# Kernel optimization log

Hardware: AMD Instinct MI355X
Metric: run time of the kernel (lower is better)

The kernel has to match this reference:

```python
import jax, jax.numpy as jnp
import numpy as np

L, B, D_IN, LATENT, H_ODE = 50, 256, 256, 512, 1024
DT = 0.1  # uniform time increment per observation


def setup_inputs() -> dict:
    key = jax.random.key(0)
    ks = jax.random.split(key, 9)
    feat = jax.random.normal(ks[0], (L, B, D_IN), dtype=jnp.float32)
    tp = jnp.full((L, B, 1), DT, dtype=jnp.float32)
    data = jnp.concatenate([feat, tp], axis=-1)  # (L, B, D_IN+1)
    hid = 2 * LATENT  # GRUCell hidden size
    s_mlp1 = 1.0 / np.sqrt(LATENT)
    s_mlp2 = 1.0 / np.sqrt(H_ODE)
    s_gru_i = 1.0 / np.sqrt(hid)
    return {
        "data": data,
        # ODE func MLP: Linear(LATENT,H_ODE) -> tanh -> Linear(H_ODE,LATENT)
        "mlp_w1": jax.random.uniform(ks[1], (LATENT, H_ODE), jnp.float32, -s_mlp1, s_mlp1),
        "mlp_b1": jax.random.uniform(ks[2], (H_ODE,), jnp.float32, -s_mlp1, s_mlp1),
        "mlp_w2": jax.random.uniform(ks[3], (H_ODE, LATENT), jnp.float32, -s_mlp2, s_mlp2),
        "mlp_b2": jax.random.uniform(ks[4], (LATENT,), jnp.float32, -s_mlp2, s_mlp2),
        # GRUCell(D_IN, hid): torch layout W_ih (3*hid, D_IN), W_hh (3*hid, hid)
        "gru_wih": jax.random.uniform(ks[5], (3 * hid, D_IN), jnp.float32, -s_gru_i, s_gru_i),
        "gru_bih": jax.random.uniform(ks[6], (3 * hid,), jnp.float32, -s_gru_i, s_gru_i),
        "gru_whh": jax.random.uniform(ks[7], (3 * hid, hid), jnp.float32, -s_gru_i, s_gru_i),
        "gru_bhh": jax.random.uniform(ks[8], (3 * hid,), jnp.float32, -s_gru_i, s_gru_i),
    }


def reference(data, mlp_w1, mlp_b1, mlp_w2, mlp_b2, gru_wih, gru_bih, gru_whh, gru_bhh):
    x_seq = data[..., :-1]          # (L, B, D_IN)
    dt_seq = data[..., -1]          # (L, B) per-step time increments
    l, bs, _ = x_seq.shape
    latent = mlp_w1.shape[0]

    # With uniform dt, minimum_step = total/200 and each step uses
    # n_intermediate_tp = floor(200/L) linspace points -> n_sub Euler substeps.
    n_tp = max(2, 200 // l)
    n_sub = n_tp - 1

    def ode_f(y):
        return jnp.tanh(y @ mlp_w1 + mlp_b1) @ mlp_w2 + mlp_b2

    def gru_cell(x, h):
        gi = x @ gru_wih.T + gru_bih
        gh = h @ gru_whh.T + gru_bhh
        ir, iz, inn = jnp.split(gi, 3, axis=-1)
        hr, hz, hn = jnp.split(gh, 3, axis=-1)
        r = jax.nn.sigmoid(ir + hr)
        z = jax.nn.sigmoid(iz + hz)
        n = jnp.tanh(inn + r * hn)
        return (1.0 - z) * n + z * h

    def step(carry, inp):
        ode_state, gru_state, _ = carry
        x, dt = inp                      # x: (B, D_IN), dt: (B,)
        h_step = (dt / n_sub)[:, None]   # Euler substep size
        y = ode_state
        for _ in range(n_sub):           # fixed small unroll
            y = y + ode_f(y) * h_step
        new_h = gru_cell(x, jnp.concatenate([y, gru_state], axis=-1))
        # Original code: ode_state = new_h[..., :latent]; gru_state = new_h[..., :-latent]
        # (both are the first `latent` dims -- faithful to the source)
        new_ode = new_h[:, :latent]
        new_gru = new_h[:, :latent]
        return (new_ode, new_gru, new_h), new_ode

    zeros_lat = jnp.zeros((bs, latent), dtype=data.dtype)
    init = (zeros_lat, zeros_lat, jnp.zeros((bs, 2 * latent), dtype=data.dtype))
    (_, _, new_h), ode_states_post = jax.lax.scan(step, init, (x_seq, dt_seq))
    return ode_states_post, new_h
```

## Files before the change

kernel.cpp:

```cpp
#include <hip/hip_runtime.h>

#define LSEQ 50
#define BATCH 256
#define DIN 256
#define LAT 512
#define HID 1024
#define ROWSTRIDE 257
#define NBLK 256

typedef __attribute__((ext_vector_type(8))) short s16x8;
typedef __attribute__((ext_vector_type(4))) float f32x4;
using u16 = unsigned short;
using u64 = unsigned long long;

__device__ __forceinline__ u16 bfhi(float v) {
  union { float f; unsigned u; } a; a.f = v;
  return (u16)((a.u + 0x7FFFu + ((a.u >> 16) & 1u)) >> 16);
}
__device__ __forceinline__ void split2(float v, u16& h, u16& l) {
  u16 hu = bfhi(v);
  union { unsigned u; float f; } hf; hf.u = ((unsigned)hu) << 16;
  h = hu; l = bfhi(v - hf.f);
}
__device__ __forceinline__ float p2f(u16 h, u16 l) {
  union { unsigned u; float f; } a, b;
  a.u = ((unsigned)h) << 16; b.u = ((unsigned)l) << 16;
  return a.f + b.f;
}
__device__ __forceinline__ float sigmoidf_(float x) { return 1.f / (1.f + __expf(-x)); }
__device__ __forceinline__ f32x4 mfma16(s16x8 a, s16x8 b, f32x4 c) {
  return __builtin_amdgcn_mfma_f32_16x16x32_bf16(a, b, c, 0, 0, 0);
}
__device__ __forceinline__ f32x4 mfma3(s16x8 ah, s16x8 al, s16x8 bh, s16x8 bl, f32x4 c) {
  c = mfma16(ah, bh, c); c = mfma16(ah, bl, c); c = mfma16(al, bh, c); return c;
}
__device__ __forceinline__ ushort4 ldu4(const u16* p) { return *(const ushort4*)p; }
__device__ __forceinline__ void stu4(u16* p, ushort4 v) { *(ushort4*)p = v; }

__device__ __forceinline__ ushort4 ldu4c(const u16* p) {
  u64 v = __hip_atomic_load((const u64*)p, __ATOMIC_RELAXED, __HIP_MEMORY_SCOPE_AGENT);
  union { u64 q; ushort4 s; } u; u.q = v; return u.s;
}
__device__ __forceinline__ u16 ldu16c(const u16* p) {
  return __hip_atomic_load(p, __ATOMIC_RELAXED, __HIP_MEMORY_SCOPE_AGENT);
}
__device__ __forceinline__ void stu16c(u16* p, u16 v) {
  __hip_atomic_store(p, v, __ATOMIC_RELAXED, __HIP_MEMORY_SCOPE_AGENT);
}

__device__ __forceinline__ void kbar() {
  asm volatile("s_waitcnt lgkmcnt(0)" ::: "memory");
  __builtin_amdgcn_s_barrier();
}

__device__ __forceinline__ void slice_barrier(unsigned* line, unsigned k) {
  asm volatile("s_waitcnt vmcnt(0)" ::: "memory");
  __syncthreads();
  if (threadIdx.x == 0) {
    __hip_atomic_fetch_add(line, 1u, __ATOMIC_RELAXED, __HIP_MEMORY_SCOPE_AGENT);
    const unsigned tgt = k * 32u;
    while (__hip_atomic_load(line, __ATOMIC_RELAXED, __HIP_MEMORY_SCOPE_AGENT) < tgt) {
      __builtin_amdgcn_s_sleep(1);
    }
  }
  __syncthreads();
}

__global__ __launch_bounds__(256) void tsplit_k(const float* __restrict__ W,
    u16* __restrict__ Thi, u16* __restrict__ Tlo, int K, int N)
{
  __shared__ unsigned Ts[32][33];
  const int bk = blockIdx.x * 32, bn = blockIdx.y * 32;
  const int t = threadIdx.x;
  const int n_l = t & 31, k_l4 = (t >> 5) * 4;
  #pragma unroll
  for (int i = 0; i < 4; i++) {
    float v = W[(size_t)(bk + k_l4 + i) * N + bn + n_l];
    u16 h, l; split2(v, h, l);
    Ts[k_l4 + i][n_l] = ((unsigned)h << 16) | l;
  }
  __syncthreads();
  const int k_l = t & 31, n_l2 = t >> 5;
  #pragma unroll
  for (int i = 0; i < 4; i++) {
    int nn = n_l2 + 8 * i;
    unsigned u = Ts[k_l][nn];
    size_t o = (size_t)(bn + nn) * K + bk + k_l;
    Thi[o] = (u16)(u >> 16);
    Tlo[o] = (u16)(u & 0xFFFFu);
  }
}

__global__ __launch_bounds__(256) void esplit_k(const float* __restrict__ W,
    u16* __restrict__ Phi, u16* __restrict__ Plo)
{
  size_t i4 = ((size_t)blockIdx.x * 256 + threadIdx.x) * 4;
  float4 v = *(const float4*)&W[i4];
  u16 h[4], l[4];
  split2(v.x, h[0], l[0]); split2(v.y, h[1], l[1]);
  split2(v.z, h[2], l[2]); split2(v.w, h[3], l[3]);
  *(ushort4*)&Phi[i4] = make_ushort4(h[0], h[1], h[2], h[3]);
  *(ushort4*)&Plo[i4] = make_ushort4(l[0], l[1], l[2], l[3]);
}

__global__ __launch_bounds__(256) void init_k(u16* __restrict__ c0h, u16* __restrict__ c0l,
                                              unsigned* __restrict__ bar)
{
  size_t i4 = ((size_t)blockIdx.x * 256 + threadIdx.x) * 4;
  *(ushort4*)&c0h[i4] = make_ushort4(0, 0, 0, 0);
  *(ushort4*)&c0l[i4] = make_ushort4(0, 0, 0, 0);
  if (blockIdx.x == 0 && threadIdx.x < 16) bar[threadIdx.x * 64] = 0u;
}

template<int EPI, int NITER>
__device__ __forceinline__ void gemm_phase(
    u16* __restrict__ Sah, u16* __restrict__ Sal,
    u16* __restrict__ Sbh, u16* __restrict__ Sbl,
    const u16* __restrict__ Ahi, const u16* __restrict__ Alo, int ldA, int m0,
    const u16* __restrict__ Bhi, const u16* __restrict__ Blo, int ldB, int n0,
    const float* __restrict__ bias,
    u16* __restrict__ Ohi, u16* __restrict__ Olo,
    const float* __restrict__ data, int t, int tid)
{
  constexpr int NSEG = NITER / 4;
  const int lane = tid & 63, wave = tid >> 6;
  const int wm = (wave >> 1) << 4, wn = (wave & 1) << 4;
  const int lr = lane & 15, lq = lane >> 4;
  const int srow = tid >> 3, sk4 = (tid & 7) << 2;
  const int sidx = srow * 40 + sk4;
  const size_t rowA = (size_t)(m0 + srow) * ldA + sk4;
  const size_t rowB = (size_t)(n0 + srow) * ldB + sk4;
  const int fa = (wm + lr) * 40 + lq * 8;
  const int fb = (wn + lr) * 40 + lq * 8;
  f32x4 acc0 = {0,0,0,0}, acc1 = {0,0,0,0};

  ushort4 ah0[4], al0[4], bh0[4], bl0[4];
  ushort4 ah1[4], al1[4], bh1[4], bl1[4];

  auto load0 = [&](int seg) {
    #pragma unroll
    for (int d = 0; d < 4; ++d) {
      const int k0 = (seg * 4 + d) << 5;
      ah0[d] = ldu4c(&Ahi[rowA + k0]); al0[d] = ldu4c(&Alo[rowA + k0]);
      bh0[d] = ldu4(&Bhi[rowB + k0]);  bl0[d] = ldu4(&Blo[rowB + k0]);
    }
  };
  auto load1 = [&](int seg) {
    #pragma unroll
    for (int d = 0; d < 4; ++d) {
      const int k0 = (seg * 4 + d) << 5;
      ah1[d] = ldu4c(&Ahi[rowA + k0]); al1[d] = ldu4c(&Alo[rowA + k0]);
      bh1[d] = ldu4(&Bhi[rowB + k0]);  bl1[d] = ldu4(&Blo[rowB + k0]);
    }
  };
  auto write0 = [&]() {
    #pragma unroll
    for (int d = 0; d < 4; ++d) {
      stu4(&Sah[d * 1280 + sidx], ah0[d]); stu4(&Sal[d * 1280 + sidx], al0[d]);
      stu4(&Sbh[d * 1280 + sidx], bh0[d]); stu4(&Sbl[d * 1280 + sidx], bl0[d]);
    }
  };
  auto write1 = [&]() {
    #pragma unroll
    for (int d = 0; d < 4; ++d) {
      stu4(&Sah[5120 + d * 1280 + sidx], ah1[d]); stu4(&Sal[5120 + d * 1280 + sidx], al1[d]);
      stu4(&Sbh[5120 + d * 1280 + sidx], bh1[d]); stu4(&Sbl[5120 + d * 1280 + sidx], bl1[d]);
    }
  };
  auto compute = [&](int g) {
    #pragma unroll
    for (int d = 0; d < 4; ++d) {
      const int o = g * 5120 + d * 1280;
      s16x8 ah = *(const s16x8*)&Sah[o + fa];
      s16x8 al = *(const s16x8*)&Sal[o + fa];
      s16x8 bh = *(const s16x8*)&Sbh[o + fb];
      s16x8 bl = *(const s16x8*)&Sbl[o + fb];
      if (d & 1) acc1 = mfma3(ah, al, bh, bl, acc1);
      else       acc0 = mfma3(ah, al, bh, bl, acc0);
    }
  };

  load0(0);
  load1(1);
  write0();
  kbar();
  for (int p = 0; p < NSEG; p += 2) {
    if (p + 2 < NSEG) load0(p + 2);
    compute(0);
    write1();
    kbar();
    if (p + 3 < NSEG) load1(p + 3);
    compute(1);
    if (p + 2 < NSEG) write0();
    kbar();
  }

  #pragma unroll
  for (int r = 0; r < 4; ++r) {
    const int row = m0 + wm + lq * 4 + r;
    const int col = n0 + wn + lr;
    float v = acc0[r] + acc1[r] + bias[col];
    size_t o = (size_t)row * HID + col;
    if (EPI == 1) {
      float h1 = tanhf(v);
      u16 h, l; split2(h1, h, l);
      stu16c(&Ohi[o], h); stu16c(&Olo[o], l);
    } else {
      float dt3 = data[(size_t)(t * BATCH + row) * ROWSTRIDE + DIN] * (1.f / 3.f);
      float y = p2f(ldu16c(&Ohi[o]), ldu16c(&Olo[o])) + v * dt3;
      u16 h, l; split2(y, h, l);
      stu16c(&Ohi[o], h); stu16c(&Olo[o], l);
    }
  }
}

template<bool PLANES>
__device__ __forceinline__ void gru_phase(
    u16* pool,
    const u16* __restrict__ chi, const u16* __restrict__ clo,
    const float* __restrict__ whh, const u16* __restrict__ whhh, const u16* __restrict__ whhl,
    const float* __restrict__ wih, const u16* __restrict__ wihh, const u16* __restrict__ wihl,
    const float* __restrict__ bih, const float* __restrict__ bhh,
    const float* __restrict__ data, int t,
    u16* __restrict__ nhi, u16* __restrict__ nlo,
    float* __restrict__ out, int gc0, int m0, int tid)
{
  u16* sAh = pool;
  u16* sAl = pool + 5120;
  u16* sBh = pool + 10240;
  u16* sBl = pool + 25600;
  const int lane = tid & 63, wave = tid >> 6;
  const int wm = (wave >> 1) << 4, wn = (wave & 1) << 4;
  const int lr = lane & 15, lq = lane >> 4;
  const int srow = tid >> 3, sk4 = (tid & 7) << 2;
  const int sidx = srow * 40 + sk4;
  const int fa = (wm + lr) * 40 + lq * 8;
  const int fbn = (wn + lr) * 40 + lq * 8;
  f32x4 aR0 = {0,0,0,0}, aR1 = {0,0,0,0};
  f32x4 aZ0 = {0,0,0,0}, aZ1 = {0,0,0,0};
  f32x4 aNh0 = {0,0,0,0}, aNh1 = {0,0,0,0};
  f32x4 aNi0 = {0,0,0,0}, aNi1 = {0,0,0,0};

  {
    const size_t rowA = (size_t)(m0 + srow) * HID + sk4;
    const size_t rB0 = (size_t)(0 * 1024 + gc0 + srow) * 1024 + sk4;
    const size_t rB1 = (size_t)(1 * 1024 + gc0 + srow) * 1024 + sk4;
    const size_t rB2 = (size_t)(2 * 1024 + gc0 + srow) * 1024 + sk4;
    ushort4 Ah0[2], Al0[2], Bh0[2][3], Bl0[2][3];
    ushort4 Ah1[2], Al1[2], Bh1[2][3], Bl1[2][3];
    float4  F0[2][3], F1[2][3];

    auto load0 = [&](int seg) {
      #pragma unroll
      for (int j = 0; j < 2; ++j) {
        const int k0 = (seg * 2 + j) << 5;
        Ah0[j] = ldu4c(&chi[rowA + k0]); Al0[j] = ldu4c(&clo[rowA + k0]);
        if (PLANES) {
          Bh0[j][0] = ldu4(&whhh[rB0 + k0]); Bl0[j][0] = ldu4(&whhl[rB0 + k0]);
          Bh0[j][1] = ldu4(&whhh[rB1 + k0]); Bl0[j][1] = ldu4(&whhl[rB1 + k0]);
          Bh0[j][2] = ldu4(&whhh[rB2 + k0]); Bl0[j][2] = ldu4(&whhl[rB2 + k0]);
        } else {
          F0[j][0] = *(const float4*)&whh[rB0 + k0];
          F0[j][1] = *(const float4*)&whh[rB1 + k0];
          F0[j][2] = *(const float4*)&whh[rB2 + k0];
        }
      }
    };
    auto load1 = [&](int seg) {
      #pragma unroll
      for (int j = 0; j < 2; ++j) {
        const int k0 = (seg * 2 + j) << 5;
        Ah1[j] = ldu4c(&chi[rowA + k0]); Al1[j] = ldu4c(&clo[rowA + k0]);
        if (PLANES) {
          Bh1[j][0] = ldu4(&whhh[rB0 + k0]); Bl1[j][0] = ldu4(&whhl[rB0 + k0]);
          Bh1[j][1] = ldu4(&whhh[rB1 + k0]); Bl1[j][1] = ldu4(&whhl[rB1 + k0]);
          Bh1[j][2] = ldu4(&whhh[rB2 + k0]); Bl1[j][2] = ldu4(&whhl[rB2 + k0]);
        } else {
          F1[j][0] = *(const float4*)&whh[rB0 + k0];
          F1[j][1] = *(const float4*)&whh[rB1 + k0];
          F1[j][2] = *(const float4*)&whh[rB2 + k0];
        }
      }
    };
    auto write0 = [&]() {
      #pragma unroll
      for (int j = 0; j < 2; ++j) {
        stu4(&sAh[j * 1280 + sidx], Ah0[j]); stu4(&sAl[j * 1280 + sidx], Al0[j]);
        #pragma unroll
        for (int g = 0; g < 3; ++g) {
          if (PLANES) {
            stu4(&sBh[j * 3840 + g * 1280 + sidx], Bh0[j][g]);
            stu4(&sBl[j * 3840 + g * 1280 + sidx], Bl0[j][g]);
          } else {
            float4 w4 = F0[j][g];
            u16 h0,l0,h1,l1,h2,l2,h3,l3;
            split2(w4.x,h0,l0); split2(w4.y,h1,l1); split2(w4.z,h2,l2); split2(w4.w,h3,l3);
            stu4(&sBh[j * 3840 + g * 1280 + sidx], make_ushort4(h0,h1,h2,h3));
            stu4(&sBl[j * 3840 + g * 1280 + sidx], make_ushort4(l0,l1,l2,l3));
          }
        }
      }
    };
    auto write1 = [&]() {
      #pragma unroll
      for (int j = 0; j < 2; ++j) {
        stu4(&sAh[(2 + j) * 1280 + sidx], Ah1[j]); stu4(&sAl[(2 + j) * 1280 + sidx], Al1[j]);
        #pragma unroll
        for (int g = 0; g < 3; ++g) {
          if (PLANES) {
            stu4(&sBh[(2 + j) * 3840 + g * 1280 + sidx], Bh1[j][g]);
            stu4(&sBl[(2 + j) * 3840 + g * 1280 + sidx], Bl1[j][g]);
          } else {
            float4 w4 = F1[j][g];
            u16 h0,l0,h1,l1,h2,l2,h3,l3;
            split2(w4.x,h0,l0); split2(w4.y,h1,l1); split2(w4.z,h2,l2); split2(w4.w,h3,l3);
            stu4(&sBh[(2 + j) * 3840 + g * 1280 + sidx], make_ushort4(h0,h1,h2,h3));
            stu4(&sBl[(2 + j) * 3840 + g * 1280 + sidx], make_ushort4(l0,l1,l2,l3));
          }
        }
      }
    };
    auto compute = [&](int grp) {
      #pragma unroll
      for (int j = 0; j < 2; ++j) {
        const int slot = grp * 2 + j;
        const int sa = slot * 1280 + fa;
        const int sb = slot * 3840 + fbn;
        s16x8 ah = *(const s16x8*)&sAh[sa];
        s16x8 al = *(const s16x8*)&sAl[sa];
        #pragma unroll
        for (int g = 0; g < 3; ++g) {
          s16x8 bh = *(const s16x8*)&sBh[sb + g * 1280];
          s16x8 bl = *(const s16x8*)&sBl[sb + g * 1280];
          if (j) {
            if (g == 0) aR1 = mfma3(ah, al, bh, bl, aR1);
            else if (g == 1) aZ1 = mfma3(ah, al, bh, bl, aZ1);
            else aNh1 = mfma3(ah, al, bh, bl, aNh1);
          } else {
            if (g == 0) aR0 = mfma3(ah, al, bh, bl, aR0);
            else if (g == 1) aZ0 = mfma3(ah, al, bh, bl, aZ0);
            else aNh0 = mfma3(ah, al, bh, bl, aNh0);
          }
        }
      }
    };

    load0(0); load1(1); write0(); kbar();
    for (int p = 0; p < 16; p += 2) {
      if (p + 2 < 16) load0(p + 2);
      compute(0);
      write1();
      kbar();
      if (p + 3 < 16) load1(p + 3);
      compute(1);
      if (p + 2 < 16) write0();
      kbar();
    }
  }

  {
    const size_t rowX = (size_t)(t * BATCH + m0 + srow) * ROWSTRIDE + sk4;
    const size_t rB0 = (size_t)(0 * 1024 + gc0 + srow) * 256 + sk4;
    const size_t rB1 = (size_t)(1 * 1024 + gc0 + srow) * 256 + sk4;
    const size_t rB2 = (size_t)(2 * 1024 + gc0 + srow) * 256 + sk4;
    float4  X0[2], X1[2];
    ushort4 Bh0[2][3], Bl0[2][3], Bh1[2][3], Bl1[2][3];
    float4  F0[2][3], F1[2][3];

    auto load0 = [&](int seg) {
      #pragma unroll
      for (int j = 0; j < 2; ++j) {
        const int k0 = (seg * 2 + j) << 5;
        X0[j] = *(const float4*)&data[rowX + k0];
        if (PLANES) {
          Bh0[j][0] = ldu4(&wihh[rB0 + k0]); Bl0[j][0] = ldu4(&wihl[rB0 + k0]);
          Bh0[j][1] = ldu4(&wihh[rB1 + k0]); Bl0[j][1] = ldu4(&wihl[rB1 + k0]);
          Bh0[j][2] = ldu4(&wihh[rB2 + k0]); Bl0[j][2] = ldu4(&wihl[rB2 + k0]);
        } else {
          F0[j][0] = *(const float4*)&wih[rB0 + k0];
          F0[j][1] = *(const float4*)&wih[rB1 + k0];
          F0[j][2] = *(const float4*)&wih[rB2 + k0];
        }
      }
    };
    auto load1 = [&](int seg) {
      #pragma unroll
      for (int j = 0; j < 2; ++j) {
        const int k0 = (seg * 2 + j) << 5;
        X1[j] = *(const float4*)&data[rowX + k0];
        if (PLANES) {
          Bh1[j][0] = ldu4(&wihh[rB0 + k0]); Bl1[j][0] = ldu4(&wihl[rB0 + k0]);
          Bh1[j][1] = ldu4(&wihh[rB1 + k0]); Bl1[j][1] = ldu4(&wihl[rB1 + k0]);
          Bh1[j][2] = ldu4(&wihh[rB2 + k0]); Bl1[j][2] = ldu4(&wihl[rB2 + k0]);
        } else {
          F1[j][0] = *(const float4*)&wih[rB0 + k0];
          F1[j][1] = *(const float4*)&wih[rB1 + k0];
          F1[j][2] = *(const float4*)&wih[rB2 + k0];
        }
      }
    };
    auto writeX = [&](const float4* X, int base) {
      #pragma unroll
      for (int j = 0; j < 2; ++j) {
        u16 xh[4], xl[4];
        split2(X[j].x, xh[0], xl[0]); split2(X[j].y, xh[1], xl[1]);
        split2(X[j].z, xh[2], xl[2]); split2(X[j].w, xh[3], xl[3]);
        stu4(&sAh[(base + j) * 1280 + sidx], make_ushort4(xh[0], xh[1], xh[2], xh[3]));
        stu4(&sAl[(base + j) * 1280 + sidx], make_ushort4(xl[0], xl[1], xl[2], xl[3]));
      }
    };
    auto write0 = [&]() {
      writeX(X0, 0);
      #pragma unroll
      for (int j = 0; j < 2; ++j)
        #pragma unroll
        for (int g = 0; g < 3; ++g) {
          if (PLANES) {
            stu4(&sBh[j * 3840 + g * 1280 + sidx], Bh0[j][g]);
            stu4(&sBl[j * 3840 + g * 1280 + sidx], Bl0[j][g]);
          } else {
            float4 w4 = F0[j][g];
            u16 h0,l0,h1,l1,h2,l2,h3,l3;
            split2(w4.x,h0,l0); split2(w4.y,h1,l1); split2(w4.z,h2,l2); split2(w4.w,h3,l3);
            stu4(&sBh[j * 3840 + g * 1280 + sidx], make_ushort4(h0,h1,h2,h3));
            stu4(&sBl[j * 3840 + g * 1280 + sidx], make_ushort4(l0,l1,l2,l3));
          }
        }
    };
    auto write1 = [&]() {
      writeX(X1, 2);
      #pragma unroll
      for (int j = 0; j < 2; ++j)
        #pragma unroll
        for (int g = 0; g < 3; ++g) {
          if (PLANES) {
            stu4(&sBh[(2 + j) * 3840 + g * 1280 + sidx], Bh1[j][g]);
            stu4(&sBl[(2 + j) * 3840 + g * 1280 + sidx], Bl1[j][g]);
          } else {
            float4 w4 = F1[j][g];
            u16 h0,l0,h1,l1,h2,l2,h3,l3;
            split2(w4.x,h0,l0); split2(w4.y,h1,l1); split2(w4.z,h2,l2); split2(w4.w,h3,l3);
            stu4(&sBh[(2 + j) * 3840 + g * 1280 + sidx], make_ushort4(h0,h1,h2,h3));
            stu4(&sBl[(2 + j) * 3840 + g * 1280 + sidx], make_ushort4(l0,l1,l2,l3));
          }
        }
    };
    auto compute = [&](int grp) {
      #pragma unroll
      for (int j = 0; j < 2; ++j) {
        const int slot = grp * 2 + j;
        const int sa = slot * 1280 + fa;
        const int sb = slot * 3840 + fbn;
        s16x8 ah = *(const s16x8*)&sAh[sa];
        s16x8 al = *(const s16x8*)&sAl[sa];
        #pragma unroll
        for (int g = 0; g < 3; ++g) {
          s16x8 bh = *(const s16x8*)&sBh[sb + g * 1280];
          s16x8 bl = *(const s16x8*)&sBl[sb + g * 1280];
          if (j) {
            if (g == 0) aR1 = mfma3(ah, al, bh, bl, aR1);
            else if (g == 1) aZ1 = mfma3(ah, al, bh, bl, aZ1);
            else aNi1 = mfma3(ah, al, bh, bl, aNi1);
          } else {
            if (g == 0) aR0 = mfma3(ah, al, bh, bl, aR0);
            else if (g == 1) aZ0 = mfma3(ah, al, bh, bl, aZ0);
            else aNi0 = mfma3(ah, al, bh, bl, aNi0);
          }
        }
      }
    };

    load0(0); load1(1); write0(); kbar();
    for (int p = 0; p < 4; p += 2) {
      if (p + 2 < 4) load0(p + 2);
      compute(0);
      write1();
      kbar();
      if (p + 3 < 4) load1(p + 3);
      compute(1);
      if (p + 2 < 4) write0();
      kbar();
    }
  }

  const f32x4 aR = aR0 + aR1, aZ = aZ0 + aZ1, aNh = aNh0 + aNh1, aNi = aNi0 + aNi1;

  #pragma unroll
  for (int r = 0; r < 4; ++r) {
    const int row = m0 + wm + lq * 4 + r;
    const int jg = gc0 + wn + lr;
    float rr = sigmoidf_(aR[r] + bih[jg] + bhh[jg]);
    float zz = sigmoidf_(aZ[r] + bih[1024 + jg] + bhh[1024 + jg]);
    float nn = tanhf(aNi[r] + bih[2048 + jg] + rr * (aNh[r] + bhh[2048 + jg]));
    size_t oh = (size_t)row * HID + jg;
    float hv = p2f(ldu16c(&chi[oh]), ldu16c(&clo[oh]));
    float val = (1.f - zz) * nn + zz * hv;
    out[(size_t)LSEQ * BATCH * LAT + oh] = val;
    if (jg < LAT) {
      out[((size_t)t * BATCH + row) * LAT + jg] = val;
      u16 h, l; split2(val, h, l);
      stu16c(&nhi[oh], h); stu16c(&nhi[oh + LAT], h);
      stu16c(&nlo[oh], l); stu16c(&nlo[oh + LAT], l);
    }
  }
}

template<bool PLANES>
__global__ __launch_bounds__(256) void fused_seq_k(
    const u16* __restrict__ w1h, const u16* __restrict__ w1l,
    const u16* __restrict__ w2h, const u16* __restrict__ w2l,
    const float* __restrict__ b1, const float* __restrict__ b2,
    u16* __restrict__ c0h, u16* __restrict__ c0l,
    u16* __restrict__ c1h, u16* __restrict__ c1l,
    u16* __restrict__ h1h, u16* __restrict__ h1l,
    const float* __restrict__ whh, const u16* __restrict__ whhh, const u16* __restrict__ whhl,
    const float* __restrict__ wih, const u16* __restrict__ wihh, const u16* __restrict__ wihl,
    const float* __restrict__ bih, const float* __restrict__ bhh,
    const float* __restrict__ data, float* __restrict__ out,
    unsigned* __restrict__ bar)
{
  __shared__ u16 pool[40960];
  const int b = blockIdx.x;
  const int tid = threadIdx.x;
  const int slice = b >> 5;
  const int l = b & 31;
  const int m0 = slice << 5;
  unsigned* line = bar + slice * 64;
  unsigned rnd = 0;

  u16* Sah = pool;
  u16* Sal = pool + 10240;
  u16* Sbh = pool + 20480;
  u16* Sbl = pool + 30720;

  for (int t = 0; t < LSEQ; ++t) {
    u16* chi = (t & 1) ? c1h : c0h;
    u16* clo = (t & 1) ? c1l : c0l;
    u16* nhi = (t & 1) ? c0h : c1h;
    u16* nlo = (t & 1) ? c0l : c1l;
    for (int s = 0; s < 3; ++s) {
      {
        const int n0 = l << 5;
        gemm_phase<1, 16>(Sah, Sal, Sbh, Sbl,
                          chi, clo, HID, m0, w1h, w1l, 512, n0,
                          b1, h1h, h1l, data, t, tid);
      }
      ++rnd; slice_barrier(line, rnd);
      if (l < 16) {
        const int n0 = l << 5;
        gemm_phase<2, 32>(Sah, Sal, Sbh, Sbl,
                          h1h, h1l, HID, m0, w2h, w2l, 1024, n0,
                          b2, chi, clo, data, t, tid);
      }
      ++rnd; slice_barrier(line, rnd);
    }
    gru_phase<PLANES>(pool, chi, clo, whh, whhh, whhl, wih, wihh, wihl,
                      bih, bhh, data, t, nhi, nlo, out, l << 5, m0, tid);
    if (t + 1 < LSEQ) { ++rnd; slice_barrier(line, rnd); }
  }
}

extern "C" void kernel_launch(void* const* d_in, const int* in_sizes, int n_in,
                              void* d_out, int out_size, void* d_ws, size_t ws_size,
                              hipStream_t stream)
{
  const float* data = (const float*)d_in[0];
  const float* w1   = (const float*)d_in[1];
  const float* b1   = (const float*)d_in[2];
  const float* w2   = (const float*)d_in[3];
  const float* b2   = (const float*)d_in[4];
  const float* wih  = (const float*)d_in[5];
  const float* bih  = (const float*)d_in[6];
  const float* whh  = (const float*)d_in[7];
  const float* bhh  = (const float*)d_in[8];
  float* out = (float*)d_out;

  char* w = (char*)d_ws;
  auto alloc = [&](size_t bytes) { char* p = w; w += bytes; return p; };
  u16* w1h = (u16*)alloc((size_t)512 * 1024 * 2);
  u16* w1l = (u16*)alloc((size_t)512 * 1024 * 2);
  u16* w2h = (u16*)alloc((size_t)512 * 1024 * 2);
  u16* w2l = (u16*)alloc((size_t)512 * 1024 * 2);
  u16* c0h = (u16*)alloc((size_t)BATCH * HID * 2);
  u16* c0l = (u16*)alloc((size_t)BATCH * HID * 2);
  u16* c1h = (u16*)alloc((size_t)BATCH * HID * 2);
  u16* c1l = (u16*)alloc((size_t)BATCH * HID * 2);
  u16* h1h = (u16*)alloc((size_t)BATCH * HID * 2);
  u16* h1l = (u16*)alloc((size_t)BATCH * HID * 2);
  unsigned* bar = (unsigned*)alloc(4096);
  size_t base = (size_t)(w - (char*)d_ws);
  size_t need_opt = base + 2 * ((size_t)3072 * 1024 * 2) + 2 * ((size_t)3072 * 256 * 2);
  bool planes = ws_size >= need_opt;
  u16 *whhh = nullptr, *whhl = nullptr, *wihh = nullptr, *wihl = nullptr;
  if (planes) {
    whhh = (u16*)alloc((size_t)3072 * 1024 * 2);
    whhl = (u16*)alloc((size_t)3072 * 1024 * 2);
    wihh = (u16*)alloc((size_t)3072 * 256 * 2);
    wihl = (u16*)alloc((size_t)3072 * 256 * 2);
  }

  tsplit_k<<<dim3(512 / 32, 1024 / 32), 256, 0, stream>>>(w1, w1h, w1l, 512, 1024);
  tsplit_k<<<dim3(1024 / 32, 512 / 32), 256, 0, stream>>>(w2, w2h, w2l, 1024, 512);
  if (planes) {
    esplit_k<<<dim3((3072 * 1024) / 1024), 256, 0, stream>>>(whh, whhh, whhl);
    esplit_k<<<dim3((3072 * 256) / 1024), 256, 0, stream>>>(wih, wihh, wihl);
  }
  init_k<<<dim3(256), 256, 0, stream>>>(c0h, c0l, bar);

  if (planes) {
    fused_seq_k<true><<<dim3(NBLK), dim3(256), 0, stream>>>(
        w1h, w1l, w2h, w2l, b1, b2, c0h, c0l, c1h, c1l, h1h, h1l,
        whh, whhh, whhl, wih, wihh, wihl, bih, bhh, data, out, bar);
  } else {
    fused_seq_k<false><<<dim3(NBLK), dim3(256), 0, stream>>>(
        w1h, w1l, w2h, w2l, b1, b2, c0h, c0l, c1h, c1l, h1h, h1l,
        whh, whhh, whhl, wih, wihh, wihl, bih, bhh, data, out, bar);
  }
}
```

Before: 4.000 ms.

## Prefetch next phase's weight tiles into registers before slice barriers

Before each inter-block slice barrier, every block issues global loads for the first weight segment of its next GEMM or GRU phase into registers. The barrier waits only for older stores (vmcnt(12)), so these prefetches stay in flight across the barrier. The next phase then takes its first B tile from registers instead of loading it after the barrier. This hides weight-load latency behind synchronisation, at the cost of extra register pressure and reliance on exact vmcnt ordering for correctness.

```diff
diff --git a/kernel.cpp b/kernel.cpp
--- a/kernel.cpp
+++ b/kernel.cpp
@@ -64,6 +64,19 @@
     }
   }
   __syncthreads();
+}
+
+__device__ __forceinline__ void slice_barrier_p12(unsigned* line, unsigned k) {
+  asm volatile("s_waitcnt vmcnt(12) lgkmcnt(0)" ::: "memory");
+  __builtin_amdgcn_s_barrier();
+  if (threadIdx.x == 0) {
+    __hip_atomic_fetch_add(line, 1u, __ATOMIC_RELAXED, __HIP_MEMORY_SCOPE_AGENT);
+    const unsigned tgt = k * 32u;
+    while (__hip_atomic_load(line, __ATOMIC_RELAXED, __HIP_MEMORY_SCOPE_AGENT) < tgt) {
+      __builtin_amdgcn_s_sleep(1);
+    }
+  }
+  __builtin_amdgcn_s_barrier();
 }
 
 __global__ __launch_bounds__(256) void tsplit_k(const float* __restrict__ W,
@@ -112,7 +125,7 @@
   if (blockIdx.x == 0 && threadIdx.x < 16) bar[threadIdx.x * 64] = 0u;
 }
 
-template<int EPI, int NITER>
+template<int EPI, int NITER, bool PRE>
 __device__ __forceinline__ void gemm_phase(
     u16* __restrict__ Sah, u16* __restrict__ Sal,
     u16* __restrict__ Sbh, u16* __restrict__ Sbl,
@@ -120,7 +133,8 @@
     const u16* __restrict__ Bhi, const u16* __restrict__ Blo, int ldB, int n0,
     const float* __restrict__ bias,
     u16* __restrict__ Ohi, u16* __restrict__ Olo,
-    const float* __restrict__ data, int t, int tid)
+    const float* __restrict__ data, int t, int tid,
+    const ushort4* preBh, const ushort4* preBl)
 {
   constexpr int NSEG = NITER / 4;
   const int lane = tid & 63, wave = tid >> 6;
@@ -180,7 +194,16 @@
     }
   };
 
-  load0(0);
+  if constexpr (PRE) {
+    #pragma unroll
+    for (int d = 0; d < 4; ++d) {
+      const int k0 = d << 5;
+      ah0[d] = ldu4c(&Ahi[rowA + k0]); al0[d] = ldu4c(&Alo[rowA + k0]);
+      bh0[d] = preBh[d]; bl0[d] = preBl[d];
+    }
+  } else {
+    load0(0);
+  }
   load1(1);
   write0();
   kbar();
@@ -223,7 +246,8 @@
     const float* __restrict__ bih, const float* __restrict__ bhh,
     const float* __restrict__ data, int t,
     u16* __restrict__ nhi, u16* __restrict__ nlo,
-    float* __restrict__ out, int gc0, int m0, int tid)
+    float* __restrict__ out, int gc0, int m0, int tid,
+    const ushort4* preBh, const ushort4* preBl)
 {
   u16* sAh = pool;
   u16* sAl = pool + 5120;
@@ -345,7 +369,18 @@
       }
     };
 
-    load0(0); load1(1); write0(); kbar();
+    if constexpr (PLANES) {
+      #pragma unroll
+      for (int j = 0; j < 2; ++j) {
+        const int k0 = j << 5;
+        Ah0[j] = ldu4c(&chi[rowA + k0]); Al0[j] = ldu4c(&clo[rowA + k0]);
+        #pragma unroll
+        for (int g = 0; g < 3; ++g) { Bh0[j][g] = preBh[j * 3 + g]; Bl0[j][g] = preBl[j * 3 + g]; }
+      }
+    } else {
+      load0(0);
+    }
+    load1(1); write0(); kbar();
     for (int p = 0; p < 16; p += 2) {
       if (p + 2 < 16) load0(p + 2);
       compute(0);
@@ -533,30 +568,95 @@
   u16* Sbh = pool + 20480;
   u16* Sbl = pool + 30720;
 
-  for (int t = 0; t < LSEQ; ++t) {
-    u16* chi = (t & 1) ? c1h : c0h;
-    u16* clo = (t & 1) ? c1l : c0l;
-    u16* nhi = (t & 1) ? c0h : c1h;
-    u16* nlo = (t & 1) ? c0l : c1l;
-    for (int s = 0; s < 3; ++s) {
-      {
-        const int n0 = l << 5;
-        gemm_phase<1, 16>(Sah, Sal, Sbh, Sbl,
-                          chi, clo, HID, m0, w1h, w1l, 512, n0,
-                          b1, h1h, h1l, data, t, tid);
-      }
-      ++rnd; slice_barrier(line, rnd);
-      if (l < 16) {
-        const int n0 = l << 5;
-        gemm_phase<2, 32>(Sah, Sal, Sbh, Sbl,
-                          h1h, h1l, HID, m0, w2h, w2l, 1024, n0,
-                          b2, chi, clo, data, t, tid);
-      }
-      ++rnd; slice_barrier(line, rnd);
-    }
-    gru_phase<PLANES>(pool, chi, clo, whh, whhh, whhl, wih, wihh, wihl,
-                      bih, bhh, data, t, nhi, nlo, out, l << 5, m0, tid);
-    if (t + 1 < LSEQ) { ++rnd; slice_barrier(line, rnd); }
+  const int srow = tid >> 3, sk4 = (tid & 7) << 2;
+  ushort4 preh[6], prel[6];
+
+  auto pre_w = [&](const u16* Bh, const u16* Bl, int ldB, int n0) {
+    size_t rowB = (size_t)(n0 + srow) * ldB + sk4;
+    #pragma unroll
+    for (int d = 0; d < 4; ++d) {
+      preh[d] = ldu4(&Bh[rowB + (d << 5)]); prel[d] = ldu4(&Bl[rowB + (d << 5)]);
+    }
+    preh[4] = ldu4(&Bh[rowB]); prel[4] = ldu4(&Bl[rowB]);
+    preh[5] = ldu4(&Bh[rowB]); prel[5] = ldu4(&Bl[rowB]);
+  };
+  auto pre_g = [&]() {
+    const int gc0 = l << 5;
+    #pragma unroll
+    for (int j = 0; j < 2; ++j)
+      #pragma unroll
+      for (int g = 0; g < 3; ++g) {
+        size_t rr = (size_t)(g * 1024 + gc0 + srow) * 1024 + (j << 5) + sk4;
+        preh[j * 3 + g] = ldu4(&whhh[rr]); prel[j * 3 + g] = ldu4(&whhl[rr]);
+      }
+  };
+
+  if constexpr (PLANES) {
+    pre_w(w1h, w1l, 512, l << 5);
+    for (int t = 0; t < LSEQ; ++t) {
+      u16* chi = (t & 1) ? c1h : c0h;
+      u16* clo = (t & 1) ? c1l : c0l;
+      u16* nhi = (t & 1) ? c0h : c1h;
+      u16* nlo = (t & 1) ? c0l : c1l;
+      for (int s = 0; s < 3; ++s) {
+        {
+          const int n0 = l << 5;
+          gemm_phase<1, 16, true>(Sah, Sal, Sbh, Sbl,
+                                  chi, clo, HID, m0, w1h, w1l, 512, n0,
+                                  b1, h1h, h1l, data, t, tid, preh, prel);
+        }
+        asm volatile("" ::: "memory");
+        if (l < 16) pre_w(w2h, w2l, 1024, l << 5);
+        else { if (s < 2) pre_w(w1h, w1l, 512, l << 5); else pre_g(); }
+        slice_barrier_p12(line, ++rnd);
+        if (l < 16) {
+          {
+            const int n0 = l << 5;
+            gemm_phase<2, 32, true>(Sah, Sal, Sbh, Sbl,
+                                    h1h, h1l, HID, m0, w2h, w2l, 1024, n0,
+                                    b2, chi, clo, data, t, tid, preh, prel);
+          }
+          asm volatile("" ::: "memory");
+          if (s < 2) pre_w(w1h, w1l, 512, l << 5); else pre_g();
+          slice_barrier_p12(line, ++rnd);
+        } else {
+          slice_barrier_p12(line, ++rnd);
+        }
+      }
+      gru_phase<true>(pool, chi, clo, whh, whhh, whhl, wih, wihh, wihl,
+                      bih, bhh, data, t, nhi, nlo, out, l << 5, m0, tid, preh, prel);
+      if (t + 1 < LSEQ) {
+        asm volatile("" ::: "memory");
+        pre_w(w1h, w1l, 512, l << 5);
+        slice_barrier_p12(line, ++rnd);
+      }
+    }
+  } else {
+    for (int t = 0; t < LSEQ; ++t) {
+      u16* chi = (t & 1) ? c1h : c0h;
+      u16* clo = (t & 1) ? c1l : c0l;
+      u16* nhi = (t & 1) ? c0h : c1h;
+      u16* nlo = (t & 1) ? c0l : c1l;
+      for (int s = 0; s < 3; ++s) {
+        {
+          const int n0 = l << 5;
+          gemm_phase<1, 16, false>(Sah, Sal, Sbh, Sbl,
+                                   chi, clo, HID, m0, w1h, w1l, 512, n0,
+                                   b1, h1h, h1l, data, t, tid, nullptr, nullptr);
+        }
+        slice_barrier(line, ++rnd);
+        if (l < 16) {
+          const int n0 = l << 5;
+          gemm_phase<2, 32, false>(Sah, Sal, Sbh, Sbl,
+                                   h1h, h1l, HID, m0, w2h, w2l, 1024, n0,
+                                   b2, chi, clo, data, t, tid, nullptr, nullptr);
+        }
+        slice_barrier(line, ++rnd);
+      }
+      gru_phase<false>(pool, chi, clo, whh, whhh, whhl, wih, wihh, wihl,
+                       bih, bhh, data, t, nhi, nlo, out, l << 5, m0, tid, nullptr, nullptr);
+      if (t + 1 < LSEQ) slice_barrier(line, ++rnd);
+    }
   }
 }
 
```

New measurement: 4.148 ms. 1.04x slower.
